# Kernel optimization log

Measured on AMD Instinct MI355X. Metric: run time of the kernel, lower is better.

The kernel has to match this reference:

```python
import jax, jax.numpy as jnp
import numpy as np

# Constant from livnium.kernel.constants (assumed scalar; value taken as 1.0).
K_O = 1.0
EPS = 1e-12  # F.normalize default eps

B, D, C = 16384, 1024, 3
F_DIM = D + 10  # features = h_final (D) + 10 scalar features


def setup_inputs() -> dict:
    key = jax.random.key(0)
    ks = jax.random.split(key, 8)
    s1 = 1.0 / np.sqrt(F_DIM)
    return {
        "h_final": jax.random.normal(ks[0], (B, D), jnp.float32),
        "v_p": jax.random.normal(ks[1], (B, D), jnp.float32),
        "v_h": jax.random.normal(ks[2], (B, D), jnp.float32),
        "neutral_dir": jax.random.normal(ks[3], (D,), jnp.float32),
        "neutral_scale": jnp.array(1.0, jnp.float32),
        "w1": jax.random.normal(ks[4], (F_DIM, F_DIM), jnp.float32) * s1,
        "b1": jnp.zeros((F_DIM,), jnp.float32),
        "w2": jax.random.normal(ks[5], (C, F_DIM), jnp.float32) * s1,
        "b2": jnp.zeros((C,), jnp.float32),
    }


def _normalize(x, axis):
    n = jnp.linalg.norm(x, axis=axis, keepdims=True)
    return x / jnp.maximum(n, EPS)


def reference(h_final, v_p, v_h, neutral_dir, neutral_scale, w1, b1, w2, b2):
    v_p_n = _normalize(v_p, -1)                      # [B, D]
    v_h_n = _normalize(v_h, -1)                      # [B, D]
    nd_n = _normalize(neutral_dir, 0)                # [D]

    # alignment(): cosine of the unit vectors == batched dot product.
    align = jnp.sum(v_p_n * v_h_n, axis=-1, keepdims=True)        # [B, 1]
    opp = jnp.sum(-v_p_n * v_h_n, axis=-1, keepdims=True)          # [B, 1]
    align_neutral_p = neutral_scale * jnp.sum(v_p_n * nd_n, axis=-1, keepdims=True)
    align_neutral_h = neutral_scale * jnp.sum(v_h_n * nd_n, axis=-1, keepdims=True)

    energy = K_O * ((1.0 + align) * 0.5)
    expose_neg = (1.0 - align) * 0.5
    dist_p_h = jnp.linalg.norm(v_h - v_p, axis=-1, keepdims=True)
    r_p = jnp.linalg.norm(v_p, axis=-1, keepdims=True)
    r_h = jnp.linalg.norm(v_h, axis=-1, keepdims=True)
    r_final = jnp.linalg.norm(h_final, axis=-1, keepdims=True)

    features = jnp.concatenate(
        [h_final, align, opp, energy, expose_neg, dist_p_h,
         r_p, r_h, r_final, align_neutral_p, align_neutral_h], axis=-1)  # [B, D+10]

    hidden = jax.nn.relu(features @ w1.T + b1)
    logits = hidden @ w2.T + b2                      # [B, C]
    return logits
```

## Files before the change

### kernel.cpp

```cpp
#include <hip/hip_runtime.h>
#include <cstdint>
#include <cstddef>

#define B_ROWS 16384
#define D_DIM  1024
#define F_REAL 1034
#define N_PAD  1152
#define K_PAD  1056
#define NK     (K_PAD / 32)
#define EPSN   1e-12f

typedef __bf16 bf16x8 __attribute__((ext_vector_type(8)));
typedef float  f32x4  __attribute__((ext_vector_type(4)));

__device__ __forceinline__ unsigned short f2bf(float f) {
    __bf16 b = (__bf16)f;
    return __builtin_bit_cast(unsigned short, b);
}

__global__ __launch_bounds__(256)
void prep_kernel(const float* __restrict__ h, const float* __restrict__ vp,
                 const float* __restrict__ vh, const float* __restrict__ nd,
                 const float* __restrict__ nsp, unsigned short* __restrict__ A)
{
    const int row  = blockIdx.x * 4 + (threadIdx.x >> 6);
    const int lane = threadIdx.x & 63;
    const float4* hp  = (const float4*)(h  + (size_t)row * D_DIM);
    const float4* vpp = (const float4*)(vp + (size_t)row * D_DIM);
    const float4* vhp = (const float4*)(vh + (size_t)row * D_DIM);
    const float4* ndp = (const float4*)nd;
    unsigned short* arow = A + (size_t)row * K_PAD;

    float s_pp = 0.f, s_hh = 0.f, s_pv = 0.f, s_ff = 0.f;
    float s_dd = 0.f, s_pn = 0.f, s_hn = 0.f, s_nn = 0.f;

    #pragma unroll
    for (int c = 0; c < 4; ++c) {
        const int idx = lane + c * 64;
        float4 p = vpp[idx], q = vhp[idx], f = hp[idx], n = ndp[idx];

        s_pp += p.x*p.x + p.y*p.y + p.z*p.z + p.w*p.w;
        s_hh += q.x*q.x + q.y*q.y + q.z*q.z + q.w*q.w;
        s_pv += p.x*q.x + p.y*q.y + p.z*q.z + p.w*q.w;
        s_ff += f.x*f.x + f.y*f.y + f.z*f.z + f.w*f.w;
        float dx = q.x-p.x, dy = q.y-p.y, dz = q.z-p.z, dw = q.w-p.w;
        s_dd += dx*dx + dy*dy + dz*dz + dw*dw;
        s_pn += p.x*n.x + p.y*n.y + p.z*n.z + p.w*n.w;
        s_hn += q.x*n.x + q.y*n.y + q.z*n.z + q.w*n.w;
        s_nn += n.x*n.x + n.y*n.y + n.z*n.z + n.w*n.w;

        ushort4 ho;
        ho.x = f2bf(f.x); ho.y = f2bf(f.y); ho.z = f2bf(f.z); ho.w = f2bf(f.w);
        *(ushort4*)(arow + idx * 4) = ho;
    }

    #pragma unroll
    for (int m = 32; m >= 1; m >>= 1) {
        s_pp += __shfl_xor(s_pp, m, 64);
        s_hh += __shfl_xor(s_hh, m, 64);
        s_pv += __shfl_xor(s_pv, m, 64);
        s_ff += __shfl_xor(s_ff, m, 64);
        s_dd += __shfl_xor(s_dd, m, 64);
        s_pn += __shfl_xor(s_pn, m, 64);
        s_hn += __shfl_xor(s_hn, m, 64);
        s_nn += __shfl_xor(s_nn, m, 64);
    }

    if (lane == 0) {
        float np_ = sqrtf(s_pp), nh_ = sqrtf(s_hh), nf = sqrtf(s_ff);
        float npc = fmaxf(np_, EPSN), nhc = fmaxf(nh_, EPSN);
        float nnc = fmaxf(sqrtf(s_nn), EPSN);
        float align = s_pv / (npc * nhc);
        float ns = nsp[0];
        unsigned short fo[32];
        fo[0] = f2bf(align);
        fo[1] = f2bf(-align);
        fo[2] = f2bf(0.5f * (1.0f + align));
        fo[3] = f2bf(0.5f * (1.0f - align));
        fo[4] = f2bf(sqrtf(s_dd));
        fo[5] = f2bf(np_);
        fo[6] = f2bf(nh_);
        fo[7] = f2bf(nf);
        fo[8] = f2bf(ns * s_pn / (npc * nnc));
        fo[9] = f2bf(ns * s_hn / (nhc * nnc));
        #pragma unroll
        for (int i = 10; i < 32; ++i) fo[i] = 0;
        #pragma unroll
        for (int i = 0; i < 8; ++i)
            *(ushort4*)(arow + D_DIM + i * 4) = *(ushort4*)(fo + i * 4);
    }
}

__global__ __launch_bounds__(256)
void convw_kernel(const float* __restrict__ w1, unsigned short* __restrict__ Bm)
{
    const int i = blockIdx.x;
    for (int j = threadIdx.x; j < K_PAD; j += 256) {
        float v = (i < F_REAL && j < F_REAL) ? w1[(size_t)i * F_REAL + j] : 0.0f;
        Bm[(size_t)i * K_PAD + j] = f2bf(v);
    }
}

__global__ __launch_bounds__(256)
void initout_kernel(const float* __restrict__ b2, float* __restrict__ out)
{
    int i = blockIdx.x * 256 + threadIdx.x;
    if (i < B_ROWS * 3) out[i] = b2[i % 3];
}

#define GLDS(g, l) __builtin_amdgcn_global_load_lds(                          \
        (const __attribute__((address_space(1))) void*)(g),                   \
        (__attribute__((address_space(3))) void*)(l), 16, 0, 0)

__global__ __launch_bounds__(256)
void gemm_kernel(const unsigned short* __restrict__ A,
                 const unsigned short* __restrict__ Bm,
                 const float* __restrict__ b1, const float* __restrict__ w2,
                 float* __restrict__ out)
{
    __shared__ __bf16 As[64 * 32];
    __shared__ __bf16 Bs[128 * 32];

    const int tid  = threadIdx.x;
    const int lane = tid & 63;
    const int wave = tid >> 6;
    const int wm = wave >> 1, wn = wave & 1;
    const int bm = blockIdx.x, bn = blockIdx.y;

    const unsigned short* ga[3];
    __bf16* la[3];
    {
        int s   = tid;
        int row = s >> 2;
        int kc  = (s & 3) ^ (row & 3);
        ga[0] = A + (size_t)(bm * 64 + row) * K_PAD + kc * 8;
        la[0] = As + s * 8;
    }
    #pragma unroll
    for (int o = 0; o < 2; ++o) {
        int s   = o * 256 + tid;
        int row = s >> 2;
        int kc  = (s & 3) ^ (row & 3);
        ga[1 + o] = Bm + (size_t)(bn * 128 + row) * K_PAD + kc * 8;
        la[1 + o] = Bs + s * 8;
    }

    const int col  = lane & 15;
    const int quad = lane >> 4;
    const int swz  = quad ^ (col & 3);
    int aoff[2], boff[4];
    #pragma unroll
    for (int i = 0; i < 2; ++i)
        aoff[i] = ((wm * 32 + i * 16 + col) * 4 + swz) * 8;
    #pragma unroll
    for (int j = 0; j < 4; ++j)
        boff[j] = ((wn * 64 + j * 16 + col) * 4 + swz) * 8;

    f32x4 acc[2][4];
    #pragma unroll
    for (int i = 0; i < 2; ++i)
        #pragma unroll
        for (int j = 0; j < 4; ++j)
            acc[i][j] = (f32x4){0.f, 0.f, 0.f, 0.f};

    for (int kt = 0; kt < NK; ++kt) {
        if (kt) __syncthreads();
        #pragma unroll
        for (int o = 0; o < 3; ++o)
            GLDS(ga[o] + kt * 32, la[o]);
        __syncthreads();

        bf16x8 av[2], bv[4];
        #pragma unroll
        for (int i = 0; i < 2; ++i) av[i] = *(const bf16x8*)(As + aoff[i]);
        #pragma unroll
        for (int j = 0; j < 4; ++j) bv[j] = *(const bf16x8*)(Bs + boff[j]);
        #pragma unroll
        for (int i = 0; i < 2; ++i)
            #pragma unroll
            for (int j = 0; j < 4; ++j)
                acc[i][j] = __builtin_amdgcn_mfma_f32_16x16x32_bf16(
                                av[i], bv[j], acc[i][j], 0, 0, 0);
    }

    float bias[4], w20[4], w21[4], w22[4];
    #pragma unroll
    for (int ni = 0; ni < 4; ++ni) {
        int n = bn * 128 + wn * 64 + ni * 16 + col;
        bool v = n < F_REAL;
        bias[ni] = v ? b1[n] : 0.0f;
        w20[ni]  = v ? w2[n] : 0.0f;
        w21[ni]  = v ? w2[F_REAL + n] : 0.0f;
        w22[ni]  = v ? w2[2 * F_REAL + n] : 0.0f;
    }
    #pragma unroll
    for (int mi = 0; mi < 2; ++mi) {
        float c0[4] = {0,0,0,0}, c1[4] = {0,0,0,0}, c2[4] = {0,0,0,0};
        #pragma unroll
        for (int ni = 0; ni < 4; ++ni) {
            #pragma unroll
            for (int r = 0; r < 4; ++r) {
                float hd = fmaxf(acc[mi][ni][r] + bias[ni], 0.0f);
                c0[r] += hd * w20[ni];
                c1[r] += hd * w21[ni];
                c2[r] += hd * w22[ni];
            }
        }
        #pragma unroll
        for (int m = 8; m >= 1; m >>= 1) {
            #pragma unroll
            for (int r = 0; r < 4; ++r) {
                c0[r] += __shfl_xor(c0[r], m, 64);
                c1[r] += __shfl_xor(c1[r], m, 64);
                c2[r] += __shfl_xor(c2[r], m, 64);
            }
        }
        if (col == 0) {
            int gm = bm * 64 + wm * 32 + mi * 16 + quad * 4;
            #pragma unroll
            for (int r = 0; r < 4; ++r) {
                atomicAdd(out + (size_t)(gm + r) * 3 + 0, c0[r]);
                atomicAdd(out + (size_t)(gm + r) * 3 + 1, c1[r]);
                atomicAdd(out + (size_t)(gm + r) * 3 + 2, c2[r]);
            }
        }
    }
}

extern "C" void kernel_launch(void* const* d_in, const int* in_sizes, int n_in,
                              void* d_out, int out_size, void* d_ws, size_t ws_size,
                              hipStream_t stream)
{
    const float* h  = (const float*)d_in[0];
    const float* vp = (const float*)d_in[1];
    const float* vh = (const float*)d_in[2];
    const float* nd = (const float*)d_in[3];
    const float* ns = (const float*)d_in[4];
    const float* w1 = (const float*)d_in[5];
    const float* b1 = (const float*)d_in[6];
    const float* w2 = (const float*)d_in[7];
    const float* b2 = (const float*)d_in[8];
    float* out = (float*)d_out;

    unsigned short* Afull = (unsigned short*)d_ws;
    unsigned short* Bfull = Afull + (size_t)B_ROWS * K_PAD;

    prep_kernel<<<B_ROWS / 4, 256, 0, stream>>>(h, vp, vh, nd, ns, Afull);
    convw_kernel<<<N_PAD, 256, 0, stream>>>(w1, Bfull);
    initout_kernel<<<(B_ROWS * 3 + 255) / 256, 256, 0, stream>>>(b2, out);
    gemm_kernel<<<dim3(B_ROWS / 64, N_PAD / 128), 256, 0, stream>>>(
        Afull, Bfull, b1, w2, out);
}
```

Measured before the change: 307.3 us.

## Register-prefetch next K-tile and double K-step to 64 in GEMM

New measurement: 299.5 us. 1.03x faster.

```diff
diff --git a/kernel.cpp b/kernel.cpp
--- a/kernel.cpp
+++ b/kernel.cpp
@@ -6,22 +6,23 @@
 #define D_DIM  1024
 #define F_REAL 1034
 #define N_PAD  1152
-#define K_PAD  1056
-#define NK     (K_PAD / 32)
+#define K_PAD  1088
+#define NK     (K_PAD / 64)
 #define EPSN   1e-12f
 
 typedef __bf16 bf16x8 __attribute__((ext_vector_type(8)));
 typedef float  f32x4  __attribute__((ext_vector_type(4)));
-
-__device__ __forceinline__ unsigned short f2bf(float f) {
+typedef unsigned short u16;
+
+__device__ __forceinline__ u16 f2bf(float f) {
     __bf16 b = (__bf16)f;
-    return __builtin_bit_cast(unsigned short, b);
+    return __builtin_bit_cast(u16, b);
 }
 
 __global__ __launch_bounds__(256)
 void prep_kernel(const float* __restrict__ h, const float* __restrict__ vp,
                  const float* __restrict__ vh, const float* __restrict__ nd,
-                 const float* __restrict__ nsp, unsigned short* __restrict__ A)
+                 const float* __restrict__ nsp, u16* __restrict__ A)
 {
     const int row  = blockIdx.x * 4 + (threadIdx.x >> 6);
     const int lane = threadIdx.x & 63;
@@ -29,7 +30,7 @@
     const float4* vpp = (const float4*)(vp + (size_t)row * D_DIM);
     const float4* vhp = (const float4*)(vh + (size_t)row * D_DIM);
     const float4* ndp = (const float4*)nd;
-    unsigned short* arow = A + (size_t)row * K_PAD;
+    u16* arow = A + (size_t)row * K_PAD;
 
     float s_pp = 0.f, s_hh = 0.f, s_pv = 0.f, s_ff = 0.f;
     float s_dd = 0.f, s_pn = 0.f, s_hn = 0.f, s_nn = 0.f;
@@ -72,7 +73,7 @@
         float nnc = fmaxf(sqrtf(s_nn), EPSN);
         float align = s_pv / (npc * nhc);
         float ns = nsp[0];
-        unsigned short fo[32];
+        u16 fo[64];
         fo[0] = f2bf(align);
         fo[1] = f2bf(-align);
         fo[2] = f2bf(0.5f * (1.0f + align));
@@ -84,15 +85,15 @@
         fo[8] = f2bf(ns * s_pn / (npc * nnc));
         fo[9] = f2bf(ns * s_hn / (nhc * nnc));
         #pragma unroll
-        for (int i = 10; i < 32; ++i) fo[i] = 0;
+        for (int i = 10; i < 64; ++i) fo[i] = 0;
         #pragma unroll
         for (int i = 0; i < 8; ++i)
-            *(ushort4*)(arow + D_DIM + i * 4) = *(ushort4*)(fo + i * 4);
-    }
-}
-
-__global__ __launch_bounds__(256)
-void convw_kernel(const float* __restrict__ w1, unsigned short* __restrict__ Bm)
+            *(uint4*)(arow + D_DIM + i * 8) = *(uint4*)(fo + i * 8);
+    }
+}
+
+__global__ __launch_bounds__(256)
+void convw_kernel(const float* __restrict__ w1, u16* __restrict__ Bm)
 {
     const int i = blockIdx.x;
     for (int j = threadIdx.x; j < K_PAD; j += 256) {
@@ -108,18 +109,14 @@
     if (i < B_ROWS * 3) out[i] = b2[i % 3];
 }
 
-#define GLDS(g, l) __builtin_amdgcn_global_load_lds(                          \
-        (const __attribute__((address_space(1))) void*)(g),                   \
-        (__attribute__((address_space(3))) void*)(l), 16, 0, 0)
-
-__global__ __launch_bounds__(256)
-void gemm_kernel(const unsigned short* __restrict__ A,
-                 const unsigned short* __restrict__ Bm,
+__global__ __launch_bounds__(256)
+void gemm_kernel(const u16* __restrict__ A,
+                 const u16* __restrict__ Bm,
                  const float* __restrict__ b1, const float* __restrict__ w2,
                  float* __restrict__ out)
 {
-    __shared__ __bf16 As[64 * 32];
-    __shared__ __bf16 Bs[128 * 32];
+    __shared__ __bf16 As[2 * 64 * 32];
+    __shared__ __bf16 Bs[2 * 128 * 32];
 
     const int tid  = threadIdx.x;
     const int lane = tid & 63;
@@ -127,22 +124,23 @@
     const int wm = wave >> 1, wn = wave & 1;
     const int bm = blockIdx.x, bn = blockIdx.y;
 
-    const unsigned short* ga[3];
-    __bf16* la[3];
+    const u16* gaA;
+    __bf16*    lA;
     {
-        int s   = tid;
-        int row = s >> 2;
-        int kc  = (s & 3) ^ (row & 3);
-        ga[0] = A + (size_t)(bm * 64 + row) * K_PAD + kc * 8;
-        la[0] = As + s * 8;
-    }
+        int row = tid >> 2;
+        int kc  = (tid & 3) ^ (row & 3);
+        gaA = A + (size_t)(bm * 64 + row) * K_PAD + kc * 8;
+        lA  = As + tid * 8;
+    }
+    const u16* gaB[2];
+    __bf16*    lB[2];
     #pragma unroll
     for (int o = 0; o < 2; ++o) {
         int s   = o * 256 + tid;
         int row = s >> 2;
         int kc  = (s & 3) ^ (row & 3);
-        ga[1 + o] = Bm + (size_t)(bn * 128 + row) * K_PAD + kc * 8;
-        la[1 + o] = Bs + s * 8;
+        gaB[o] = Bm + (size_t)(bn * 128 + row) * K_PAD + kc * 8;
+        lB[o]  = Bs + s * 8;
     }
 
     const int col  = lane & 15;
@@ -163,24 +161,59 @@
         for (int j = 0; j < 4; ++j)
             acc[i][j] = (f32x4){0.f, 0.f, 0.f, 0.f};
 
+    uint4 ra0, ra1, rb00, rb01, rb10, rb11;
+    ra0  = *(const uint4*)(gaA);
+    ra1  = *(const uint4*)(gaA + 32);
+    rb00 = *(const uint4*)(gaB[0]);
+    rb01 = *(const uint4*)(gaB[0] + 32);
+    rb10 = *(const uint4*)(gaB[1]);
+    rb11 = *(const uint4*)(gaB[1] + 32);
+    *(uint4*)(lA)            = ra0;
+    *(uint4*)(lA + 2048)     = ra1;
+    *(uint4*)(lB[0])         = rb00;
+    *(uint4*)(lB[0] + 4096)  = rb01;
+    *(uint4*)(lB[1])         = rb10;
+    *(uint4*)(lB[1] + 4096)  = rb11;
+    __syncthreads();
+
     for (int kt = 0; kt < NK; ++kt) {
-        if (kt) __syncthreads();
-        #pragma unroll
-        for (int o = 0; o < 3; ++o)
-            GLDS(ga[o] + kt * 32, la[o]);
-        __syncthreads();
-
-        bf16x8 av[2], bv[4];
-        #pragma unroll
-        for (int i = 0; i < 2; ++i) av[i] = *(const bf16x8*)(As + aoff[i]);
-        #pragma unroll
-        for (int j = 0; j < 4; ++j) bv[j] = *(const bf16x8*)(Bs + boff[j]);
-        #pragma unroll
-        for (int i = 0; i < 2; ++i)
-            #pragma unroll
-            for (int j = 0; j < 4; ++j)
-                acc[i][j] = __builtin_amdgcn_mfma_f32_16x16x32_bf16(
-                                av[i], bv[j], acc[i][j], 0, 0, 0);
+        if (kt + 1 < NK) {
+            const int ko = (kt + 1) * 64;
+            ra0  = *(const uint4*)(gaA + ko);
+            ra1  = *(const uint4*)(gaA + ko + 32);
+            rb00 = *(const uint4*)(gaB[0] + ko);
+            rb01 = *(const uint4*)(gaB[0] + ko + 32);
+            rb10 = *(const uint4*)(gaB[1] + ko);
+            rb11 = *(const uint4*)(gaB[1] + ko + 32);
+        }
+
+        #pragma unroll
+        for (int h = 0; h < 2; ++h) {
+            const __bf16* Ab = As + h * 2048;
+            const __bf16* Bb = Bs + h * 4096;
+            bf16x8 av[2], bv[4];
+            #pragma unroll
+            for (int i = 0; i < 2; ++i) av[i] = *(const bf16x8*)(Ab + aoff[i]);
+            #pragma unroll
+            for (int j = 0; j < 4; ++j) bv[j] = *(const bf16x8*)(Bb + boff[j]);
+            #pragma unroll
+            for (int i = 0; i < 2; ++i)
+                #pragma unroll
+                for (int j = 0; j < 4; ++j)
+                    acc[i][j] = __builtin_amdgcn_mfma_f32_16x16x32_bf16(
+                                    av[i], bv[j], acc[i][j], 0, 0, 0);
+        }
+
+        if (kt + 1 < NK) {
+            __syncthreads();
+            *(uint4*)(lA)            = ra0;
+            *(uint4*)(lA + 2048)     = ra1;
+            *(uint4*)(lB[0])         = rb00;
+            *(uint4*)(lB[0] + 4096)  = rb01;
+            *(uint4*)(lB[1])         = rb10;
+            *(uint4*)(lB[1] + 4096)  = rb11;
+            __syncthreads();
+        }
     }
 
     float bias[4], w20[4], w21[4], w22[4];
@@ -242,8 +275,8 @@
     const float* b2 = (const float*)d_in[8];
     float* out = (float*)d_out;
 
-    unsigned short* Afull = (unsigned short*)d_ws;
-    unsigned short* Bfull = Afull + (size_t)B_ROWS * K_PAD;
+    u16* Afull = (u16*)d_ws;
+    u16* Bfull = Afull + (size_t)B_ROWS * K_PAD;
 
     prep_kernel<<<B_ROWS / 4, 256, 0, stream>>>(h, vp, vh, nd, ns, Afull);
     convw_kernel<<<N_PAD, 256, 0, stream>>>(w1, Bfull);
```
